# Kernel optimization log

Measured on AMD Instinct MI355X. Metric: run time of the kernel, lower is better.

The kernel has to match this reference:

```python
import jax, jax.numpy as jnp
import numpy as np

B, N, C_CLASS, C_CHARGE, S_MAX = 128, 256, 5, 3, 300


def setup_inputs() -> dict:
    key = jax.random.key(0)
    ks = jax.random.split(key, 12)
    return {
        "particle_class": jax.random.randint(ks[0], (B, N), 0, C_CLASS),
        "particle_charge": jax.random.randint(ks[1], (B, N), 0, C_CHARGE),
        "n_particles": jax.random.randint(ks[2], (B,), 0, S_MAX),
        "pflow_class_logits": jax.random.normal(ks[3], (B, N, C_CLASS), jnp.float32),
        "pflow_charge_logits": jax.random.normal(ks[4], (B, N, C_CHARGE), jnp.float32),
        "particle_pos": jax.random.normal(ks[5], (B, N, 3), jnp.float32),
        "pflow_pos": jax.random.normal(ks[6], (B, N, 3), jnp.float32),
        "particle_mom": jax.random.normal(ks[7], (B, N, 3), jnp.float32),
        "pflow_mom": jax.random.normal(ks[8], (B, N, 3), jnp.float32),
        "particle_energy": jax.random.normal(ks[9], (B, N), jnp.float32),
        "pflow_energy": jax.random.normal(ks[10], (B, N), jnp.float32),
        "predicted_setsizes": jax.random.normal(ks[11], (B, N, S_MAX), jnp.float32),
    }


def _pairwise_nll(logits, labels):
    # logits: [B, Nq, C] (pflow/dst side), labels: [B, Np] int (particle/src side)
    # returns CE(dst_logits_j, src_label_i) for every pair -> [B, Np, Nq]
    logp = jax.nn.log_softmax(logits, axis=-1)            # [B, Nq, C]
    idx = labels[:, :, None, None]                        # [B, Np, 1, 1]
    return -jnp.take_along_axis(logp[:, None, :, :], idx, axis=3)[..., 0]


def reference(particle_class, particle_charge, n_particles,
              pflow_class_logits, pflow_charge_logits,
              particle_pos, pflow_pos, particle_mom, pflow_mom,
              particle_energy, pflow_energy, predicted_setsizes):
    # per-edge (full bipartite per event) pair losses -> [B, Np, Nq]
    class_l = _pairwise_nll(pflow_class_logits, particle_class)
    charge_l = _pairwise_nll(pflow_charge_logits, particle_charge)
    pos_l = jnp.linalg.norm(particle_pos[:, :, None, :] - pflow_pos[:, None, :, :], axis=-1)
    mom_l = jnp.linalg.norm(particle_mom[:, :, None, :] - pflow_mom[:, None, :, :], axis=-1)
    en_l = (particle_energy[:, :, None] - pflow_energy[:, None, :]) ** 2
    pair_loss = class_l + charge_l + pos_l + mom_l + en_l  # [B, Np, Nq]

    # segment-min over mailbox: per-pflow min over incoming particle edges,
    # per-particle min over incoming pflow edges
    min_per_pflow = pair_loss.min(axis=1)      # [B, Nq]
    min_per_particle = pair_loss.min(axis=2)   # [B, Np]

    particle_loss = min_per_particle.sum(axis=1).mean()
    pflow_loss = min_per_pflow.sum(axis=1).mean()

    # setsize: mean over pflow nodes per event, CE against true multiplicity
    setsize_logp = jax.nn.log_softmax(predicted_setsizes.mean(axis=1), axis=-1)  # [B, S]
    setsize_loss = -jnp.take_along_axis(setsize_logp, n_particles[:, None], axis=1)[:, 0].mean()

    loss = particle_loss + pflow_loss + setsize_loss
    return loss
```

## Files before the change

### kernel.cpp

```cpp
#include <hip/hip_runtime.h>
#include <math.h>

#define BQ 128
#define NQ 256
#define SMAX 300
#define SPAD 304
#define CCLS 5
#define CCHG 3
#define TSTR 268
#define RSTR 12
#define INFV 3.0e38f

#define NPAIR 256
#define NMAIN 512

__device__ __forceinline__ float fast_sqrtf(float x) {
    return __builtin_amdgcn_sqrtf(x);
}

#define P_TAB   0
#define P_COLS  4020
#define P_ROWS  6068
#define P_RED   7604
#define P_PART  9652
#define SMEM_FLOATS 9656

#define WS_SS 65536

__global__ __launch_bounds__(512, 2) void main_kernel(
    const int* __restrict__ p_class, const int* __restrict__ p_charge,
    const float* __restrict__ cls_logits, const float* __restrict__ chg_logits,
    const float* __restrict__ p_pos, const float* __restrict__ pf_pos,
    const float* __restrict__ p_mom, const float* __restrict__ pf_mom,
    const float* __restrict__ p_en, const float* __restrict__ pf_en,
    const float* __restrict__ setsizes, float* __restrict__ ws,
    float* __restrict__ out)
{
    __shared__ float smem[SMEM_FLOATS];
    const int t = threadIdx.x;
    const int blk = blockIdx.x;

    if (blk < NPAIR) {
        const int b  = blk >> 1;
        const int rh = blk & 1;
        const int base = b * NQ;
        float* s_tab  = smem + P_TAB;
        float* s_cols = smem + P_COLS;
        float* s_rows = smem + P_ROWS;
        float* s_red  = smem + P_RED;
        float* s_part = smem + P_PART;

        if (t < NQ) {
            const int gj = base + t;
            const float* cl = cls_logits + (size_t)gj * CCLS;
            float l0=cl[0], l1=cl[1], l2=cl[2], l3=cl[3], l4=cl[4];
            float mx = fmaxf(fmaxf(fmaxf(l0,l1),fmaxf(l2,l3)),l4);
            float lse = mx + __logf(__expf(l0-mx)+__expf(l1-mx)+__expf(l2-mx)+
                                    __expf(l3-mx)+__expf(l4-mx));
            const float* gl = chg_logits + (size_t)gj * CCHG;
            float g0=gl[0], g1=gl[1], g2=gl[2];
            float gmx = fmaxf(fmaxf(g0,g1),g2);
            float glse = gmx + __logf(__expf(g0-gmx)+__expf(g1-gmx)+__expf(g2-gmx));
            float nc[CCLS] = {lse-l0, lse-l1, lse-l2, lse-l3, lse-l4};
            float ng[CCHG] = {glse-g0, glse-g1, glse-g2};
            #pragma unroll
            for (int c = 0; c < CCLS; ++c)
                #pragma unroll
                for (int g = 0; g < CCHG; ++g)
                    s_tab[(c*CCHG+g)*TSTR + t] = nc[c] + ng[g];

            float* cr = &s_cols[t*8];
            cr[0]=pf_pos[gj*3+0]; cr[1]=pf_pos[gj*3+1]; cr[2]=pf_pos[gj*3+2];
            cr[3]=pf_mom[gj*3+0]; cr[4]=pf_mom[gj*3+1]; cr[5]=pf_mom[gj*3+2];
            cr[6]=pf_en[gj];      cr[7]=0.0f;
        } else if (t < NQ + 128) {
            const int rr = t - NQ;
            const int gr = base + rh*128 + rr;
            float* rw = &s_rows[rr*RSTR];
            rw[0]=p_pos[gr*3+0]; rw[1]=p_pos[gr*3+1]; rw[2]=p_pos[gr*3+2];
            rw[3]=p_mom[gr*3+0]; rw[4]=p_mom[gr*3+1]; rw[5]=p_mom[gr*3+2];
            rw[6]=p_en[gr];
            rw[7]=__int_as_float(p_class[gr]*CCHG + p_charge[gr]);
        }
        __syncthreads();

        const int tx = t & 31;
        const int ty = t >> 5;
        const int c0 = ty * 16;

        float4 ra[4], rb[4];
        int ccr[4];
        #pragma unroll
        for (int r = 0; r < 4; ++r) {
            const int row = tx + 32*r;
            ra[r] = *(const float4*)&s_rows[row*RSTR];
            rb[r] = *(const float4*)&s_rows[row*RSTR + 4];
            ccr[r] = __float_as_int(rb[r].w) * TSTR;
        }
        float cmin[16];
        #pragma unroll
        for (int c = 0; c < 16; ++c) cmin[c] = INFV;
        float rmin[4] = {INFV, INFV, INFV, INFV};

        #pragma unroll 4
        for (int c = 0; c < 16; ++c) {
            const int j = c0 + c;
            const float4 cd0 = *(const float4*)&s_cols[j*8];
            const float4 cd1 = *(const float4*)&s_cols[j*8+4];
            float cm = cmin[c];
            #pragma unroll
            for (int r = 0; r < 4; ++r) {
                float dx=ra[r].x-cd0.x, dy=ra[r].y-cd0.y, dz=ra[r].z-cd0.z;
                float ex=ra[r].w-cd0.w, ey=rb[r].x-cd1.x, ez=rb[r].y-cd1.y;
                float de=rb[r].z-cd1.z;
                float v = s_tab[ccr[r] + j]
                        + fast_sqrtf(dx*dx + dy*dy + dz*dz)
                        + fast_sqrtf(ex*ex + ey*ey + ez*ez)
                        + de*de;
                rmin[r] = fminf(rmin[r], v);
                cm = fminf(cm, v);
            }
            cmin[c] = cm;
        }

        #pragma unroll 4
        for (int c = 0; c < 16; ++c) {
            float v = cmin[c];
            #pragma unroll
            for (int off = 16; off > 0; off >>= 1)
                v = fminf(v, __shfl_down(v, off, 32));
            if (tx == 0) ws[blk*NQ + c0 + c] = v;
        }
        #pragma unroll
        for (int r = 0; r < 4; ++r)
            s_red[ty*128 + tx + 32*r] = rmin[r];
        __syncthreads();

        if (t < 128) {
            float m = s_red[t];
            #pragma unroll
            for (int k = 1; k < 16; ++k) m = fminf(m, s_red[k*128 + t]);
            #pragma unroll
            for (int off = 32; off > 0; off >>= 1) m += __shfl_down(m, off, 64);
            if ((t & 63) == 0) s_part[t >> 6] = m;
        }
        __syncthreads();
        if (t == 0)
            atomicAdd(out, (s_part[0] + s_part[1]) * (1.0f / BQ));

    } else {
        const int sblk = blk - NPAIR;
        const int b  = sblk >> 1;
        const int h  = sblk & 1;
        if (t < SMAX) {
            const float* p = setsizes + ((size_t)b * NQ + (size_t)h * 128) * SMAX + t;
            float acc = 0.f;
            #pragma unroll 16
            for (int i = 0; i < 128; ++i) acc += p[(size_t)i * SMAX];
            ws[WS_SS + sblk * SPAD + t] = acc;
        }
    }
}

__global__ __launch_bounds__(512) void finish_kernel(
    const float* __restrict__ ws, const int* __restrict__ n_particles,
    float* __restrict__ out)
{
    const int b = blockIdx.x;
    const int t = threadIdx.x;
    __shared__ float s_m[SPAD];
    __shared__ float s_p[8];
    __shared__ float s_cs[1];
    __shared__ float s_one[1];
    const int wave = t >> 6, lane = t & 63;

    float v = 0.f;
    if (t < NQ)
        v = fminf(ws[(b*2)*NQ + t], ws[(b*2+1)*NQ + t]);
    #pragma unroll
    for (int off = 32; off > 0; off >>= 1) v += __shfl_down(v, off, 64);
    if (lane == 0 && wave < 4) s_p[wave] = v;
    __syncthreads();
    if (t == 0) s_cs[0] = s_p[0] + s_p[1] + s_p[2] + s_p[3];
    __syncthreads();

    float m = -INFV;
    if (t < SMAX) {
        const float* p = ws + WS_SS + (size_t)(b*2) * SPAD + t;
        m = (p[0] + p[SPAD]) * (1.0f / NQ);
        s_m[t] = m;
    }
    float wm = m;
    #pragma unroll
    for (int off = 32; off > 0; off >>= 1) wm = fmaxf(wm, __shfl_down(wm, off, 64));
    if (lane == 0 && wave < 5) s_p[wave] = wm;
    __syncthreads();
    if (t == 0)
        s_one[0] = fmaxf(fmaxf(fmaxf(s_p[0], s_p[1]), fmaxf(s_p[2], s_p[3])), s_p[4]);
    __syncthreads();
    const float mx = s_one[0];
    float e = (t < SMAX) ? __expf(m - mx) : 0.f;
    #pragma unroll
    for (int off = 32; off > 0; off >>= 1) e += __shfl_down(e, off, 64);
    __syncthreads();
    if (lane == 0 && wave < 5) s_p[wave] = e;
    __syncthreads();
    if (t == 0) {
        float s = s_p[0] + s_p[1] + s_p[2] + s_p[3] + s_p[4];
        int nb = n_particles[b];
        float loss = -(s_m[nb] - mx - __logf(s));
        atomicAdd(out, (s_cs[0] + loss) * (1.0f / BQ));
    }
}

extern "C" void kernel_launch(void* const* d_in, const int* in_sizes, int n_in,
                              void* d_out, int out_size, void* d_ws, size_t ws_size,
                              hipStream_t stream) {
    (void)in_sizes; (void)n_in; (void)ws_size;
    const int*   p_class     = (const int*)d_in[0];
    const int*   p_charge    = (const int*)d_in[1];
    const int*   n_particles = (const int*)d_in[2];
    const float* cls_logits  = (const float*)d_in[3];
    const float* chg_logits  = (const float*)d_in[4];
    const float* p_pos       = (const float*)d_in[5];
    const float* pf_pos      = (const float*)d_in[6];
    const float* p_mom       = (const float*)d_in[7];
    const float* pf_mom      = (const float*)d_in[8];
    const float* p_en        = (const float*)d_in[9];
    const float* pf_en       = (const float*)d_in[10];
    const float* setsizes    = (const float*)d_in[11];
    float* out = (float*)d_out;
    float* ws  = (float*)d_ws;

    (void)hipMemsetAsync(out, 0, sizeof(float) * (size_t)out_size, stream);

    main_kernel<<<NMAIN, 512, 0, stream>>>(
        p_class, p_charge, cls_logits, chg_logits,
        p_pos, pf_pos, p_mom, pf_mom, p_en, pf_en, setsizes, ws, out);

    finish_kernel<<<BQ, 512, 0, stream>>>(ws, n_particles, out);
}
```

Baseline: 113.1 us.

## Fuse finish kernel into main kernel via per-event atomic ticket counter

Result: slower. 147.0 us (+29.9%).

```diff
diff --git a/kernel.cpp b/kernel.cpp
--- a/kernel.cpp
+++ b/kernel.cpp
@@ -25,10 +25,12 @@
 #define P_PART  9652
 #define SMEM_FLOATS 9656
 
-#define WS_SS 65536
+#define WS_SS   65536
+#define WS_TICK (WS_SS + 256*SPAD)
 
 __global__ __launch_bounds__(512, 2) void main_kernel(
     const int* __restrict__ p_class, const int* __restrict__ p_charge,
+    const int* __restrict__ n_particles,
     const float* __restrict__ cls_logits, const float* __restrict__ chg_logits,
     const float* __restrict__ p_pos, const float* __restrict__ pf_pos,
     const float* __restrict__ p_mom, const float* __restrict__ pf_mom,
@@ -37,11 +39,13 @@
     float* __restrict__ out)
 {
     __shared__ float smem[SMEM_FLOATS];
+    __shared__ int s_tick;
     const int t = threadIdx.x;
     const int blk = blockIdx.x;
+    int b;
 
     if (blk < NPAIR) {
-        const int b  = blk >> 1;
+        b = blk >> 1;
         const int rh = blk & 1;
         const int base = b * NQ;
         float* s_tab  = smem + P_TAB;
@@ -150,8 +154,8 @@
 
     } else {
         const int sblk = blk - NPAIR;
-        const int b  = sblk >> 1;
-        const int h  = sblk & 1;
+        b = sblk >> 1;
+        const int h = sblk & 1;
         if (t < SMAX) {
             const float* p = setsizes + ((size_t)b * NQ + (size_t)h * 128) * SMAX + t;
             float acc = 0.f;
@@ -159,19 +163,20 @@
             for (int i = 0; i < 128; ++i) acc += p[(size_t)i * SMAX];
             ws[WS_SS + sblk * SPAD + t] = acc;
         }
-    }
-}
-
-__global__ __launch_bounds__(512) void finish_kernel(
-    const float* __restrict__ ws, const int* __restrict__ n_particles,
-    float* __restrict__ out)
-{
-    const int b = blockIdx.x;
-    const int t = threadIdx.x;
-    __shared__ float s_m[SPAD];
-    __shared__ float s_p[8];
-    __shared__ float s_cs[1];
-    __shared__ float s_one[1];
+        __syncthreads();
+    }
+
+    if (t == 0) {
+        __threadfence();
+        s_tick = atomicAdd((int*)ws + WS_TICK + b, 1);
+    }
+    __syncthreads();
+    if (s_tick != 3) return;
+    __threadfence();
+
+    float* f_m   = smem;
+    float* f_p   = smem + 304;
+    float* f_one = smem + 312;
     const int wave = t >> 6, lane = t & 63;
 
     float v = 0.f;
@@ -179,37 +184,38 @@
         v = fminf(ws[(b*2)*NQ + t], ws[(b*2+1)*NQ + t]);
     #pragma unroll
     for (int off = 32; off > 0; off >>= 1) v += __shfl_down(v, off, 64);
-    if (lane == 0 && wave < 4) s_p[wave] = v;
-    __syncthreads();
-    if (t == 0) s_cs[0] = s_p[0] + s_p[1] + s_p[2] + s_p[3];
+    __syncthreads();
+    if (lane == 0 && wave < 4) f_p[wave] = v;
+    __syncthreads();
+    const float colsum = f_p[0] + f_p[1] + f_p[2] + f_p[3];
     __syncthreads();
 
     float m = -INFV;
     if (t < SMAX) {
         const float* p = ws + WS_SS + (size_t)(b*2) * SPAD + t;
         m = (p[0] + p[SPAD]) * (1.0f / NQ);
-        s_m[t] = m;
+        f_m[t] = m;
     }
     float wm = m;
     #pragma unroll
     for (int off = 32; off > 0; off >>= 1) wm = fmaxf(wm, __shfl_down(wm, off, 64));
-    if (lane == 0 && wave < 5) s_p[wave] = wm;
+    if (lane == 0 && wave < 5) f_p[wave] = wm;
     __syncthreads();
     if (t == 0)
-        s_one[0] = fmaxf(fmaxf(fmaxf(s_p[0], s_p[1]), fmaxf(s_p[2], s_p[3])), s_p[4]);
-    __syncthreads();
-    const float mx = s_one[0];
+        f_one[0] = fmaxf(fmaxf(fmaxf(f_p[0], f_p[1]), fmaxf(f_p[2], f_p[3])), f_p[4]);
+    __syncthreads();
+    const float mx = f_one[0];
     float e = (t < SMAX) ? __expf(m - mx) : 0.f;
     #pragma unroll
     for (int off = 32; off > 0; off >>= 1) e += __shfl_down(e, off, 64);
     __syncthreads();
-    if (lane == 0 && wave < 5) s_p[wave] = e;
+    if (lane == 0 && wave < 5) f_p[wave] = e;
     __syncthreads();
     if (t == 0) {
-        float s = s_p[0] + s_p[1] + s_p[2] + s_p[3] + s_p[4];
+        float s = f_p[0] + f_p[1] + f_p[2] + f_p[3] + f_p[4];
         int nb = n_particles[b];
-        float loss = -(s_m[nb] - mx - __logf(s));
-        atomicAdd(out, (s_cs[0] + loss) * (1.0f / BQ));
+        float loss = -(f_m[nb] - mx - __logf(s));
+        atomicAdd(out, (colsum + loss) * (1.0f / BQ));
     }
 }
 
@@ -233,10 +239,9 @@
     float* ws  = (float*)d_ws;
 
     (void)hipMemsetAsync(out, 0, sizeof(float) * (size_t)out_size, stream);
+    (void)hipMemsetAsync(ws + WS_TICK, 0, BQ * sizeof(int), stream);
 
     main_kernel<<<NMAIN, 512, 0, stream>>>(
-        p_class, p_charge, cls_logits, chg_logits,
+        p_class, p_charge, n_particles, cls_logits, chg_logits,
         p_pos, pf_pos, p_mom, pf_mom, p_en, pf_en, setsizes, ws, out);
-
-    finish_kernel<<<BQ, 512, 0, stream>>>(ws, n_particles, out);
 }
```
